# Kernel optimization log

Hardware: AMD Instinct MI355X
Metric: run time of the kernel (lower is better)

Reference implementation:

```python
import jax, jax.numpy as jnp
import numpy as np

IN_FEATURES = 8192
OUT_FEATURES = 8192
CODESZ = 8            # E8 lattice dimension per code index
CODEBOOK_SIZE = 65536 # 2^16-entry codebook (16-bit indices)
TOKENS = 32           # decode-style batch


def fwht(x):
    """Fast Walsh-Hadamard transform (Sylvester order) along the last axis.
    n must be a power of 2. Unnormalized (multiply by H_n)."""
    n = x.shape[-1]
    steps = int(np.log2(n))
    h = 1
    for _ in range(steps):
        y = x.reshape(*x.shape[:-1], n // (2 * h), 2, h)
        a = y[..., 0, :]
        b = y[..., 1, :]
        x = jnp.stack([a + b, a - b], axis=-2).reshape(*y.shape[:-3], n)
        h *= 2
    return x


def setup_inputs() -> dict:
    key = jax.random.key(0)
    k0, k1, k2, k3, k4 = jax.random.split(key, 5)
    x = jax.random.normal(k0, (TOKENS, IN_FEATURES), dtype=jnp.float32)
    # learned codebook: CODEBOOK_SIZE vectors of CODESZ entries (E8P-like lattice points)
    codebook_table = jax.random.normal(k1, (CODEBOOK_SIZE, CODESZ), dtype=jnp.float32) * 0.1
    # quantized weight indices: [out_features, in_features // codesz]
    Qidxs = jax.random.randint(k2, (OUT_FEATURES, IN_FEATURES // CODESZ), 0, CODEBOOK_SIZE, dtype=jnp.int32)
    # random sign vectors (incoherence processing)
    SU = (2.0 * jax.random.randint(k3, (IN_FEATURES,), 0, 2) - 1.0).astype(jnp.float32)
    SV = (2.0 * jax.random.randint(k4, (OUT_FEATURES,), 0, 2) - 1.0).astype(jnp.float32)
    Wscale = jnp.array(0.02, dtype=jnp.float32)
    return {"x": x, "codebook_table": codebook_table, "Qidxs": Qidxs,
            "SU": SU, "SV": SV, "Wscale": Wscale}


def reference(x, codebook_table, Qidxs, SU, SV, Wscale):
    n_in = x.shape[-1]
    n_out = SV.shape[0]
    # input incoherence: sign flip then orthonormal Hadamard rotation (matmul_hadUt)
    xh = fwht(x * SU) * (1.0 / jnp.sqrt(jnp.float32(n_in)))  # [T, n_in]
    # codebook dequantization: gather lattice vectors and lay out as [n_out, n_in]
    W = codebook_table[Qidxs].reshape(n_out, n_in)
    # quantized matmul in the rotated basis
    z = xh @ W.T  # [T, n_out]
    # output rotation (matmul_hadU) + sign/scale (SV absorbs Wscale in the torch code)
    out = fwht(z) * (1.0 / jnp.sqrt(jnp.float32(n_out))) * (SV * Wscale)
    return out
```

## Files before the change

kernel.cpp:

```cpp
#include <hip/hip_runtime.h>
#include <hip/hip_bf16.h>


typedef __attribute__((ext_vector_type(4))) float f32x4;
typedef __attribute__((ext_vector_type(8))) __bf16 bf16x8;
typedef __attribute__((ext_vector_type(4))) __bf16 bf16x4;

#define IN_F 8192
#define OUT_F 8192
#define TOKENS 32
#define KSPLIT 4
#define KCHUNK (IN_F / KSPLIT)
#define NKT (KCHUNK / 32)
#define INV_SQRT_8192 0.011048543456039806f

__global__ void cvt_cb_kernel(const float* __restrict__ cb,
                              __bf16* __restrict__ out) {
    int i = blockIdx.x * blockDim.x + threadIdx.x;
    const float4* in4 = (const float4*)cb;
    float4 v = in4[i];
    bf16x4 o;
    o[0] = (__bf16)v.x; o[1] = (__bf16)v.y;
    o[2] = (__bf16)v.z; o[3] = (__bf16)v.w;
    ((bf16x4*)out)[i] = o;
}

__global__ void had_in_kernel(const float* __restrict__ x,
                              const float* __restrict__ su,
                              __bf16* __restrict__ xh) {
    __shared__ float s[IN_F];
    const int t = blockIdx.x;
    const int tid = threadIdx.x;
    #pragma unroll
    for (int i = tid; i < IN_F; i += 1024)
        s[i] = x[t * IN_F + i] * su[i];
    __syncthreads();
    for (int h = 1; h < IN_F; h <<= 1) {
        #pragma unroll
        for (int b = 0; b < 4; ++b) {
            int j = tid + b * 1024;
            int p = ((j & ~(h - 1)) << 1) | (j & (h - 1));
            float a = s[p], c = s[p + h];
            s[p] = a + c;
            s[p + h] = a - c;
        }
        __syncthreads();
    }
    #pragma unroll
    for (int i = tid; i < IN_F; i += 1024)
        xh[t * IN_F + i] = (__bf16)(s[i] * INV_SQRT_8192);
}

__global__ __launch_bounds__(256, 2)
void qgemm_kernel(const int* __restrict__ qidxs,
                  const __bf16* __restrict__ cb,
                  const __bf16* __restrict__ xh,
                  float* __restrict__ zpart) {
    const int ks   = blockIdx.x & (KSPLIT - 1);
    const int nb   = blockIdx.x >> 2;
    const int wave = threadIdx.x >> 6;
    const int lane = threadIdx.x & 63;
    const int quad = lane >> 4;
    const int l16  = lane & 15;
    const int n = nb * 64 + wave * 16 + l16;

    const int* qrow = qidxs + n * (IN_F / 8) + ks * (KCHUNK / 8);
    const bf16x8* a0p = (const bf16x8*)(xh + l16 * IN_F + ks * KCHUNK + quad * 8);
    const bf16x8* a1p = (const bf16x8*)(xh + (l16 + 16) * IN_F + ks * KCHUNK + quad * 8);
    const bf16x8* cbv = (const bf16x8*)cb;

    f32x4 acc0 = {0.f, 0.f, 0.f, 0.f};
    f32x4 acc1 = {0.f, 0.f, 0.f, 0.f};

    #pragma unroll 4
    for (int kt = 0; kt < NKT; ++kt) {
        int idx = qrow[kt * 4 + quad];
        bf16x8 b = cbv[idx];
        bf16x8 a0 = a0p[kt * 4];
        bf16x8 a1 = a1p[kt * 4];
        acc0 = __builtin_amdgcn_mfma_f32_16x16x32_bf16(a0, b, acc0, 0, 0, 0);
        acc1 = __builtin_amdgcn_mfma_f32_16x16x32_bf16(a1, b, acc1, 0, 0, 0);
    }

    float* zp = zpart + (size_t)ks * TOKENS * OUT_F + n;
    #pragma unroll
    for (int r = 0; r < 4; ++r) {
        zp[(quad * 4 + r) * OUT_F] = acc0[r];
        zp[(16 + quad * 4 + r) * OUT_F] = acc1[r];
    }
}

__global__ void had_out_kernel(const float* __restrict__ zpart,
                               const float* __restrict__ sv,
                               const float* __restrict__ wscale,
                               float* __restrict__ out) {
    __shared__ float s[OUT_F];
    const int t = blockIdx.x;
    const int tid = threadIdx.x;
    #pragma unroll
    for (int i = tid; i < OUT_F; i += 1024) {
        float acc = 0.f;
        #pragma unroll
        for (int ks = 0; ks < KSPLIT; ++ks)
            acc += zpart[((size_t)ks * TOKENS + t) * OUT_F + i];
        s[i] = acc;
    }
    __syncthreads();
    for (int h = 1; h < OUT_F; h <<= 1) {
        #pragma unroll
        for (int b = 0; b < 4; ++b) {
            int j = tid + b * 1024;
            int p = ((j & ~(h - 1)) << 1) | (j & (h - 1));
            float a = s[p], c = s[p + h];
            s[p] = a + c;
            s[p + h] = a - c;
        }
        __syncthreads();
    }
    const float sc = INV_SQRT_8192 * wscale[0];
    #pragma unroll
    for (int i = tid; i < OUT_F; i += 1024)
        out[t * OUT_F + i] = s[i] * sc * sv[i];
}

extern "C" void kernel_launch(void* const* d_in, const int* in_sizes, int n_in,
                              void* d_out, int out_size, void* d_ws, size_t ws_size,
                              hipStream_t stream) {
    const float* x      = (const float*)d_in[0];
    const float* cb     = (const float*)d_in[1];
    const int*   qidxs  = (const int*)d_in[2];
    const float* su     = (const float*)d_in[3];
    const float* sv     = (const float*)d_in[4];
    const float* wscale = (const float*)d_in[5];
    float* out = (float*)d_out;

    char* ws = (char*)d_ws;
    __bf16* cb_bf16 = (__bf16*)ws;
    __bf16* xh      = (__bf16*)(ws + (1u << 20));
    float*  zpart   = (float*)(ws + (1u << 20) + (512u << 10));

    hipLaunchKernelGGL(cvt_cb_kernel, dim3(512), dim3(256), 0, stream,
                       cb, cb_bf16);
    hipLaunchKernelGGL(had_in_kernel, dim3(TOKENS), dim3(1024), 0, stream,
                       x, su, xh);
    hipLaunchKernelGGL(qgemm_kernel, dim3(128 * KSPLIT), dim3(256), 0, stream,
                       qidxs, cb_bf16, xh, zpart);
    hipLaunchKernelGGL(had_out_kernel, dim3(TOKENS), dim3(1024), 0, stream,
                       zpart, sv, wscale, out);
}
```

Before: 156.8 us.

## Fuse prep kernels, register-blocked FWHT, prefetch indices, raise k-split

```diff
diff --git a/kernel.cpp b/kernel.cpp
--- a/kernel.cpp
+++ b/kernel.cpp
@@ -9,62 +9,109 @@
 #define IN_F 8192
 #define OUT_F 8192
 #define TOKENS 32
-#define KSPLIT 4
-#define KCHUNK (IN_F / KSPLIT)
-#define NKT (KCHUNK / 32)
 #define INV_SQRT_8192 0.011048543456039806f
 
-__global__ void cvt_cb_kernel(const float* __restrict__ cb,
-                              __bf16* __restrict__ out) {
-    int i = blockIdx.x * blockDim.x + threadIdx.x;
-    const float4* in4 = (const float4*)cb;
-    float4 v = in4[i];
-    bf16x4 o;
-    o[0] = (__bf16)v.x; o[1] = (__bf16)v.y;
-    o[2] = (__bf16)v.z; o[3] = (__bf16)v.w;
-    ((bf16x4*)out)[i] = o;
-}
-
-__global__ void had_in_kernel(const float* __restrict__ x,
-                              const float* __restrict__ su,
-                              __bf16* __restrict__ xh) {
-    __shared__ float s[IN_F];
-    const int t = blockIdx.x;
+#define PAD(i) ((i) + ((i) >> 5))
+
+__device__ inline void fwht32_reg(float* r) {
+    #pragma unroll
+    for (int h = 1; h < 32; h <<= 1) {
+        #pragma unroll
+        for (int i = 0; i < 32; i += 2 * h) {
+            #pragma unroll
+            for (int j = 0; j < h; ++j) {
+                float a = r[i + j], b = r[i + j + h];
+                r[i + j] = a + b;
+                r[i + j + h] = a - b;
+            }
+        }
+    }
+}
+
+__device__ inline void fwht8192_lds(float* s, int tid) {
+    float r[32];
+    int b1 = tid * 32;
+    #pragma unroll
+    for (int j = 0; j < 32; ++j) r[j] = s[PAD(b1 + j)];
+    fwht32_reg(r);
+    #pragma unroll
+    for (int j = 0; j < 32; ++j) s[PAD(b1 + j)] = r[j];
+    __syncthreads();
+    int b2 = (tid & 31) + (tid >> 5) * 1024;
+    #pragma unroll
+    for (int j = 0; j < 32; ++j) r[j] = s[PAD(b2 + 32 * j)];
+    fwht32_reg(r);
+    #pragma unroll
+    for (int j = 0; j < 32; ++j) s[PAD(b2 + 32 * j)] = r[j];
+    __syncthreads();
+    #pragma unroll
+    for (int jj = 0; jj < 4; ++jj) {
+        float g[8];
+        int b3 = tid * 4 + jj;
+        #pragma unroll
+        for (int k = 0; k < 8; ++k) g[k] = s[PAD(b3 + 1024 * k)];
+        #pragma unroll
+        for (int h = 1; h < 8; h <<= 1) {
+            #pragma unroll
+            for (int i = 0; i < 8; i += 2 * h) {
+                #pragma unroll
+                for (int j = 0; j < h; ++j) {
+                    float a = g[i + j], b = g[i + j + h];
+                    g[i + j] = a + b;
+                    g[i + j + h] = a - b;
+                }
+            }
+        }
+        #pragma unroll
+        for (int k = 0; k < 8; ++k) s[PAD(b3 + 1024 * k)] = g[k];
+    }
+    __syncthreads();
+}
+
+__global__ __launch_bounds__(256)
+void prep_kernel(const float* __restrict__ cb, __bf16* __restrict__ cbb,
+                 const float* __restrict__ x, const float* __restrict__ su,
+                 __bf16* __restrict__ xh) {
+    __shared__ float s[8192 + 256];
     const int tid = threadIdx.x;
-    #pragma unroll
-    for (int i = tid; i < IN_F; i += 1024)
-        s[i] = x[t * IN_F + i] * su[i];
-    __syncthreads();
-    for (int h = 1; h < IN_F; h <<= 1) {
-        #pragma unroll
-        for (int b = 0; b < 4; ++b) {
-            int j = tid + b * 1024;
-            int p = ((j & ~(h - 1)) << 1) | (j & (h - 1));
-            float a = s[p], c = s[p + h];
-            s[p] = a + c;
-            s[p + h] = a - c;
-        }
-        __syncthreads();
-    }
-    #pragma unroll
-    for (int i = tid; i < IN_F; i += 1024)
-        xh[t * IN_F + i] = (__bf16)(s[i] * INV_SQRT_8192);
-}
-
-__global__ __launch_bounds__(256, 2)
+    if (blockIdx.x < 512) {
+        int i = blockIdx.x * 256 + tid;
+        float4 v = ((const float4*)cb)[i];
+        bf16x4 o;
+        o[0] = (__bf16)v.x; o[1] = (__bf16)v.y;
+        o[2] = (__bf16)v.z; o[3] = (__bf16)v.w;
+        ((bf16x4*)cbb)[i] = o;
+        return;
+    }
+    const int t = blockIdx.x - 512;
+    #pragma unroll
+    for (int i = tid; i < IN_F; i += 256)
+        s[PAD(i)] = x[t * IN_F + i] * su[i];
+    __syncthreads();
+    fwht8192_lds(s, tid);
+    #pragma unroll
+    for (int i = tid; i < IN_F; i += 256)
+        xh[t * IN_F + i] = (__bf16)(s[PAD(i)] * INV_SQRT_8192);
+}
+
+template <int KS>
+__global__ __launch_bounds__(256, 4)
 void qgemm_kernel(const int* __restrict__ qidxs,
                   const __bf16* __restrict__ cb,
                   const __bf16* __restrict__ xh,
                   float* __restrict__ zpart) {
-    const int ks   = blockIdx.x & (KSPLIT - 1);
-    const int nb   = blockIdx.x >> 2;
+    constexpr int KCHUNK = IN_F / KS;
+    constexpr int NKT = KCHUNK / 32;
+    constexpr int G = NKT / 8;
+    const int ks   = blockIdx.x % KS;
+    const int nb   = blockIdx.x / KS;
     const int wave = threadIdx.x >> 6;
     const int lane = threadIdx.x & 63;
     const int quad = lane >> 4;
     const int l16  = lane & 15;
     const int n = nb * 64 + wave * 16 + l16;
 
-    const int* qrow = qidxs + n * (IN_F / 8) + ks * (KCHUNK / 8);
+    const int* qp = qidxs + (size_t)n * (IN_F / 8) + ks * (KCHUNK / 8);
     const bf16x8* a0p = (const bf16x8*)(xh + l16 * IN_F + ks * KCHUNK + quad * 8);
     const bf16x8* a1p = (const bf16x8*)(xh + (l16 + 16) * IN_F + ks * KCHUNK + quad * 8);
     const bf16x8* cbv = (const bf16x8*)cb;
@@ -72,14 +119,26 @@
     f32x4 acc0 = {0.f, 0.f, 0.f, 0.f};
     f32x4 acc1 = {0.f, 0.f, 0.f, 0.f};
 
-    #pragma unroll 4
-    for (int kt = 0; kt < NKT; ++kt) {
-        int idx = qrow[kt * 4 + quad];
-        bf16x8 b = cbv[idx];
-        bf16x8 a0 = a0p[kt * 4];
-        bf16x8 a1 = a1p[kt * 4];
-        acc0 = __builtin_amdgcn_mfma_f32_16x16x32_bf16(a0, b, acc0, 0, 0, 0);
-        acc1 = __builtin_amdgcn_mfma_f32_16x16x32_bf16(a1, b, acc1, 0, 0, 0);
+    int idx[8];
+    #pragma unroll
+    for (int j = 0; j < 8; ++j) idx[j] = qp[j * 4 + quad];
+
+    #pragma unroll 1
+    for (int g = 0; g < G; ++g) {
+        const int po = (g + 1 < G ? g + 1 : g) * 32;
+        int nidx[8];
+        #pragma unroll
+        for (int j = 0; j < 8; ++j) nidx[j] = qp[po + j * 4 + quad];
+        #pragma unroll
+        for (int j = 0; j < 8; ++j) {
+            bf16x8 b = cbv[idx[j]];
+            bf16x8 a0 = a0p[(g * 8 + j) * 4];
+            bf16x8 a1 = a1p[(g * 8 + j) * 4];
+            acc0 = __builtin_amdgcn_mfma_f32_16x16x32_bf16(a0, b, acc0, 0, 0, 0);
+            acc1 = __builtin_amdgcn_mfma_f32_16x16x32_bf16(a1, b, acc1, 0, 0, 0);
+        }
+        #pragma unroll
+        for (int j = 0; j < 8; ++j) idx[j] = nidx[j];
     }
 
     float* zp = zpart + (size_t)ks * TOKENS * OUT_F + n;
@@ -90,37 +149,29 @@
     }
 }
 
-__global__ void had_out_kernel(const float* __restrict__ zpart,
-                               const float* __restrict__ sv,
-                               const float* __restrict__ wscale,
-                               float* __restrict__ out) {
-    __shared__ float s[OUT_F];
+template <int KS>
+__global__ __launch_bounds__(256)
+void had_out_kernel(const float* __restrict__ zpart,
+                    const float* __restrict__ sv,
+                    const float* __restrict__ wscale,
+                    float* __restrict__ out) {
+    __shared__ float s[8192 + 256];
     const int t = blockIdx.x;
     const int tid = threadIdx.x;
     #pragma unroll
-    for (int i = tid; i < OUT_F; i += 1024) {
+    for (int i = tid; i < OUT_F; i += 256) {
         float acc = 0.f;
         #pragma unroll
-        for (int ks = 0; ks < KSPLIT; ++ks)
-            acc += zpart[((size_t)ks * TOKENS + t) * OUT_F + i];
-        s[i] = acc;
-    }
-    __syncthreads();
-    for (int h = 1; h < OUT_F; h <<= 1) {
-        #pragma unroll
-        for (int b = 0; b < 4; ++b) {
-            int j = tid + b * 1024;
-            int p = ((j & ~(h - 1)) << 1) | (j & (h - 1));
-            float a = s[p], c = s[p + h];
-            s[p] = a + c;
-            s[p + h] = a - c;
-        }
-        __syncthreads();
-    }
+        for (int k = 0; k < KS; ++k)
+            acc += zpart[((size_t)k * TOKENS + t) * OUT_F + i];
+        s[PAD(i)] = acc;
+    }
+    __syncthreads();
+    fwht8192_lds(s, tid);
     const float sc = INV_SQRT_8192 * wscale[0];
     #pragma unroll
-    for (int i = tid; i < OUT_F; i += 1024)
-        out[t * OUT_F + i] = s[i] * sc * sv[i];
+    for (int i = tid; i < OUT_F; i += 256)
+        out[t * OUT_F + i] = s[PAD(i)] * sc * sv[i];
 }
 
 extern "C" void kernel_launch(void* const* d_in, const int* in_sizes, int n_in,
@@ -139,12 +190,21 @@
     __bf16* xh      = (__bf16*)(ws + (1u << 20));
     float*  zpart   = (float*)(ws + (1u << 20) + (512u << 10));
 
-    hipLaunchKernelGGL(cvt_cb_kernel, dim3(512), dim3(256), 0, stream,
-                       cb, cb_bf16);
-    hipLaunchKernelGGL(had_in_kernel, dim3(TOKENS), dim3(1024), 0, stream,
-                       x, su, xh);
-    hipLaunchKernelGGL(qgemm_kernel, dim3(128 * KSPLIT), dim3(256), 0, stream,
-                       qidxs, cb_bf16, xh, zpart);
-    hipLaunchKernelGGL(had_out_kernel, dim3(TOKENS), dim3(1024), 0, stream,
-                       zpart, sv, wscale, out);
-}
+    const size_t need8 = (1u << 20) + (512u << 10) +
+                         (size_t)8 * TOKENS * OUT_F * 4;
+    const bool big = ws_size >= need8;
+
+    hipLaunchKernelGGL(prep_kernel, dim3(544), dim3(256), 0, stream,
+                       cb, cb_bf16, x, su, xh);
+    if (big) {
+        hipLaunchKernelGGL((qgemm_kernel<8>), dim3(128 * 8), dim3(256), 0,
+                           stream, qidxs, cb_bf16, xh, zpart);
+        hipLaunchKernelGGL((had_out_kernel<8>), dim3(TOKENS), dim3(256), 0,
+                           stream, zpart, sv, wscale, out);
+    } else {
+        hipLaunchKernelGGL((qgemm_kernel<4>), dim3(128 * 4), dim3(256), 0,
+                           stream, qidxs, cb_bf16, xh, zpart);
+        hipLaunchKernelGGL((had_out_kernel<4>), dim3(TOKENS), dim3(256), 0,
+                           stream, zpart, sv, wscale, out);
+    }
+}
```

Result: slower. 160.0 us (+2.0%).
